# Performance work log

Hardware: AMD Instinct MI355X
Metric: run time of the kernel (lower is better)

The kernel has to match this reference:

```python
import jax, jax.numpy as jnp
import numpy as np

K = 32            # config.k: active latents per token (batch top-k)
THRESHOLD_LR = 0.01
B, S, F = 8, 256, 16384


def setup_inputs() -> dict:
    key = jax.random.key(0)
    k1, k2 = jax.random.split(key)
    x = jax.random.normal(k1, (B, S, F), dtype=jnp.float32)
    token_mask = jax.random.randint(k2, (B, S), 0, 2, dtype=jnp.int32)
    threshold = jnp.zeros((), dtype=jnp.float32)  # persistent EMA buffer, init 0.0
    return {"x": x, "token_mask": token_mask, "threshold": threshold}


def reference(x, token_mask, threshold):
    # Training path of BatchTopKActivationFunction.forward
    b, s, f = x.shape
    num_tokens = b * s
    k_total = K * num_tokens
    neg_min = jnp.finfo(x.dtype).min
    # mask out tokens: x[~token_mask] = finfo.min (so they never enter top-k)
    xm = jnp.where(token_mask.astype(bool)[:, :, None], x, neg_min)
    flat = xm.reshape(-1)                       # [b*s*f]
    vals, idx = jax.lax.top_k(flat, k_total)    # global top-k over flattened tensor
    # scatter relu'd top-k values back into a zero tensor
    result = jnp.zeros_like(flat).at[idx].set(jax.nn.relu(vals)).reshape(b, s, f)
    # EMA threshold update: min of strictly-positive selected values
    pos = vals > 0
    min_pos = jnp.min(jnp.where(pos, vals, jnp.inf))
    new_threshold = jnp.where(
        jnp.any(pos),
        (1.0 - THRESHOLD_LR) * threshold + THRESHOLD_LR * min_pos,
        threshold,
    )
    return result, new_threshold
```

## Files before the change

### kernel.cpp

```cpp
#include <hip/hip_runtime.h>

#define N_ELEMS  33554432
#define N4       8388608
#define N_TOKENS 2048
#define F4       4096
#define K_TOTAL  65536u
#define NBINS    4096

#define C_NG       4096
#define C_WINTH    4097
#define C_CANDTH   4098
#define C_NEED     4099
#define C_FB       4100
#define C_N2       4101
#define N_CTR_END  4160

#define GLIST_OFF  8192u
#define CAPG       4194304u
#define LIST2_OFF  (GLIST_OFF + 2u*CAPG)
#define CAP2       4096u
#define FB1_OFF    16777216u
#define CAPF       2097152u
#define FB2_OFF    (FB1_OFF + 2u*CAPF)

__device__ __forceinline__ unsigned keyOf(float f) {
    unsigned b = __float_as_uint(f);
    return b ^ ((unsigned)((int)b >> 31) | 0x80000000u);
}
__device__ __forceinline__ float valOf(unsigned u) {
    unsigned b = (u & 0x80000000u) ? (u ^ 0x80000000u) : ~u;
    return __uint_as_float(b);
}
__device__ __forceinline__ unsigned umaxu(unsigned a, unsigned b) { return a > b ? a : b; }

__global__ void k_init(unsigned* __restrict__ ws) {
    int t = blockIdx.x * 256 + threadIdx.x;
    if (t < N_CTR_END) ws[t] = 0u;
}

#define GBUF 1024
__global__ __launch_bounds__(512) void k_hist(const float4* __restrict__ x,
                                              const int* __restrict__ mask,
                                              unsigned* __restrict__ ws,
                                              float4* __restrict__ out) {
    __shared__ unsigned lh[NBINS];
    __shared__ uint2 sbuf[GBUF];
    __shared__ unsigned s_cnt, s_base;
    const int tok = blockIdx.x;
    float4* ot = out + (size_t)tok * F4;
    const float4 z = make_float4(0.f, 0.f, 0.f, 0.f);
    if (!mask[tok]) {
        for (int j = threadIdx.x; j < F4; j += 512) ot[j] = z;
        return;
    }
    for (int b = threadIdx.x; b < NBINS; b += 512) lh[b] = 0u;
    if (threadIdx.x == 0) s_cnt = 0u;
    __syncthreads();
    uint2* glist = (uint2*)(ws + GLIST_OFF);
    const float4* xt = x + (size_t)tok * F4;
    const unsigned baseIdx = (unsigned)tok * 16384u;
    for (int j = threadIdx.x; j < F4; j += 512) {
        float4 v = xt[j];
        ot[j] = z;
        float fv[4] = {v.x, v.y, v.z, v.w};
        #pragma unroll
        for (int c = 0; c < 4; c++) {
            float f = fv[c];
            if (f >= 2.0f) {
                unsigned u = keyOf(f);
                unsigned bin = (u - 0xC0000000u) >> 12;
                if (bin > 4095u) bin = 4095u;
                atomicAdd(&lh[bin], 1u);
                unsigned slot = atomicAdd(&s_cnt, 1u);
                uint2 e = make_uint2(u, baseIdx + (unsigned)j * 4u + (unsigned)c);
                if (slot < GBUF) sbuf[slot] = e;
                else { unsigned g = atomicAdd(&ws[C_NG], 1u); if (g < CAPG) glist[g] = e; }
            }
        }
    }
    __syncthreads();
    for (int b = threadIdx.x; b < NBINS; b += 512) {
        unsigned c = lh[b];
        if (c) atomicAdd(&ws[b], c);
    }
    unsigned cnt = s_cnt; if (cnt > GBUF) cnt = GBUF;
    if (threadIdx.x == 0) s_base = atomicAdd(&ws[C_NG], cnt);
    __syncthreads();
    for (unsigned j = threadIdx.x; j < cnt; j += 512) {
        unsigned p = s_base + j;
        if (p < CAPG) glist[p] = sbuf[j];
    }
}

__global__ __launch_bounds__(1024) void k_scan1(unsigned* __restrict__ ws) {
    __shared__ unsigned sc[1024];
    __shared__ unsigned sB1, sKA, sFound;
    const int t = threadIdx.x;
    unsigned vv[4];
    unsigned s = 0u;
    #pragma unroll
    for (int j = 0; j < 4; ++j) { vv[j] = ws[t * 4 + j]; s += vv[j]; }
    if (t == 0) sFound = 0u;
    sc[t] = s;
    __syncthreads();
    for (int off = 1; off < 1024; off <<= 1) {
        unsigned a = sc[t];
        unsigned b = (t + off < 1024) ? sc[t + off] : 0u;
        __syncthreads();
        sc[t] = a + b;
        __syncthreads();
    }
    unsigned run = (t < 1023) ? sc[t + 1] : 0u;
    #pragma unroll
    for (int j = 3; j >= 0; --j) {
        unsigned prev = run; run += vv[j];
        if (run >= K_TOTAL && prev < K_TOTAL) {
            sB1 = (unsigned)(t * 4 + j); sKA = prev; sFound = 1u;
        }
    }
    __syncthreads();
    if (t == 0) {
        unsigned total = sc[0];
        unsigned ng = ws[C_NG];
        unsigned fb = (sFound == 0u) || (total < K_TOTAL) || (sB1 == 4095u) || (ng > CAPG);
        ws[C_FB] = fb ? 1u : 0u;
        if (!fb) {
            unsigned candTh = 0xC0000000u + (sB1 << 12);
            ws[C_CANDTH] = candTh;
            ws[C_WINTH]  = candTh + 0x1000u;
            ws[C_NEED]   = K_TOTAL - sKA;
        }
    }
}

__global__ __launch_bounds__(256) void k_scatter(unsigned* __restrict__ ws,
                                                 float* __restrict__ out) {
    if (ws[C_FB]) return;
    const unsigned winTh = ws[C_WINTH], candTh = ws[C_CANDTH];
    unsigned ng = ws[C_NG]; if (ng > CAPG) ng = CAPG;
    uint2* glist = (uint2*)(ws + GLIST_OFF);
    uint2* list2 = (uint2*)(ws + LIST2_OFF);
    const unsigned stride = gridDim.x * 256;
    for (unsigned i = blockIdx.x * 256 + threadIdx.x; i < ng; i += stride) {
        uint2 e = glist[i];
        if (e.x >= winTh) out[e.y] = valOf(e.x);
        else if (e.x >= candTh) {
            unsigned g = atomicAdd(&ws[C_N2], 1u);
            if (g < CAP2) list2[g] = e;
        }
    }
}

__global__ __launch_bounds__(256) void k_tail(unsigned* __restrict__ ws,
                                              float* __restrict__ out,
                                              const float* __restrict__ thr) {
    if (ws[C_FB]) return;
    __shared__ uint2 ent[CAP2];
    __shared__ unsigned sred[256];
    const int t = threadIdx.x;
    unsigned rawn2 = ws[C_N2];
    if (rawn2 > CAP2) { if (t == 0) ws[C_FB] = 1u; return; }
    const unsigned n2 = rawn2;
    const unsigned need = ws[C_NEED];
    uint2* list2 = (uint2*)(ws + LIST2_OFF);
    for (unsigned i = t; i < n2; i += 256) ent[i] = list2[i];
    __syncthreads();
    unsigned minSel = 0xFFFFFFFFu;
    for (unsigned i = t; i < n2; i += 256) {
        uint2 e = ent[i];
        unsigned rank = 0u;
        for (unsigned j = 0; j < n2; ++j) {
            uint2 o = ent[j];
            rank += (o.x > e.x || (o.x == e.x && o.y < e.y)) ? 1u : 0u;
        }
        if (rank < need) {
            out[e.y] = valOf(e.x);
            if (e.x < minSel) minSel = e.x;
        }
    }
    sred[t] = minSel;
    __syncthreads();
    for (int off = 128; off > 0; off >>= 1) {
        if (t < off) sred[t] = sred[t] < sred[t + off] ? sred[t] : sred[t + off];
        __syncthreads();
    }
    if (t == 0) {
        out[N_ELEMS] = 0.99f * thr[0] + 0.01f * valOf(sred[0]);
    }
}

__global__ __launch_bounds__(1024) void k_fallback(const float4* __restrict__ x,
                                                   const int* __restrict__ mask,
                                                   unsigned* __restrict__ ws,
                                                   float* __restrict__ out,
                                                   const float* __restrict__ thr) {
    if (ws[C_FB] == 0u) return;
    __shared__ unsigned lh[NBINS];
    __shared__ unsigned sred[1024];
    __shared__ unsigned sB1, sKA, sMode, sNegmin, sB2, sNeed, sCnt;
    const int t = threadIdx.x;
    for (int b = t; b < NBINS; b += 1024) lh[b] = 0u;
    __syncthreads();
    unsigned negmin = 0u;
    for (int tok = 0; tok < N_TOKENS; ++tok) {
        if (!mask[tok]) continue;
        const float4* xt = x + (size_t)tok * F4;
        for (int j = t; j < F4; j += 1024) {
            float4 v = xt[j];
            float fv[4] = {v.x, v.y, v.z, v.w};
            #pragma unroll
            for (int c = 0; c < 4; ++c) {
                float f = fv[c];
                unsigned u = keyOf(f);
                atomicAdd(&lh[u >> 20], 1u);
                if (f > 0.0f) negmin = umaxu(negmin, ~u);
            }
        }
    }
    __syncthreads();
    sred[t] = negmin; __syncthreads();
    for (int off = 512; off > 0; off >>= 1) {
        if (t < off) sred[t] = umaxu(sred[t], sred[t + off]);
        __syncthreads();
    }
    if (t == 0) {
        sNegmin = sred[0];
        unsigned tot = 0u;
        for (int b = 0; b < NBINS; ++b) tot += lh[b];
        if (tot <= K_TOTAL) sMode = 1u;
        else {
            sMode = 0u;
            unsigned run = 0u, prev = 0u; int b1 = 0;
            for (int b = NBINS - 1; b >= 0; --b) {
                prev = run; run += lh[b];
                if (run >= K_TOTAL && prev < K_TOTAL) { b1 = b; break; }
            }
            sB1 = (unsigned)b1; sKA = prev;
        }
        sCnt = 0u;
    }
    __syncthreads();
    if (sMode == 1u) {
        for (int tok = 0; tok < N_TOKENS; ++tok) {
            if (!mask[tok]) continue;
            const float4* xt = x + (size_t)tok * F4;
            float* ot = out + (size_t)tok * 16384;
            for (int j = t; j < F4; j += 1024) {
                float4 v = xt[j];
                ot[j * 4 + 0] = fmaxf(v.x, 0.f); ot[j * 4 + 1] = fmaxf(v.y, 0.f);
                ot[j * 4 + 2] = fmaxf(v.z, 0.f); ot[j * 4 + 3] = fmaxf(v.w, 0.f);
            }
        }
        if (t == 0) {
            float th = thr[0], newt = th;
            if (sNegmin) newt = 0.99f * th + 0.01f * valOf(~sNegmin);
            out[N_ELEMS] = newt;
        }
        return;
    }
    const unsigned B1c = sB1;
    uint2* fb1 = (uint2*)(ws + FB1_OFF);
    for (int tok = 0; tok < N_TOKENS; ++tok) {
        if (!mask[tok]) continue;
        const float4* xt = x + (size_t)tok * F4;
        const unsigned baseIdx = (unsigned)tok * 16384u;
        for (int j = t; j < F4; j += 1024) {
            float4 v = xt[j];
            float fv[4] = {v.x, v.y, v.z, v.w};
            #pragma unroll
            for (int c = 0; c < 4; ++c) {
                float f = fv[c];
                unsigned u = keyOf(f);
                unsigned p = u >> 20;
                unsigned idx = baseIdx + (unsigned)j * 4u + (unsigned)c;
                if (p > B1c) out[idx] = fmaxf(f, 0.f);
                else if (p == B1c) {
                    unsigned g = atomicAdd(&sCnt, 1u);
                    if (g < CAPF) fb1[g] = make_uint2(u, idx);
                }
            }
        }
    }
    __syncthreads();
    unsigned n1 = sCnt > CAPF ? CAPF : sCnt;
    __syncthreads();
    if (t < 256) lh[t] = 0u;
    if (t == 0) sCnt = 0u;
    __syncthreads();
    for (unsigned i = t; i < n1; i += 1024)
        atomicAdd(&lh[(fb1[i].x >> 12) & 255u], 1u);
    __syncthreads();
    if (t == 0) {
        unsigned run = sKA, prev = sKA; int b2 = 0;
        for (int b = 255; b >= 0; --b) {
            prev = run; run += lh[b];
            if (run >= K_TOTAL) { b2 = b; break; }
        }
        sB2 = (unsigned)b2; sNeed = K_TOTAL - prev;
    }
    __syncthreads();
    const unsigned B2 = sB2, need = sNeed;
    uint2* fb2 = (uint2*)(ws + FB2_OFF);
    for (unsigned i = t; i < n1; i += 1024) {
        uint2 e = fb1[i];
        unsigned bb = (e.x >> 12) & 255u;
        if (bb > B2) out[e.y] = fmaxf(valOf(e.x), 0.f);
        else if (bb == B2) {
            unsigned g = atomicAdd(&sCnt, 1u);
            if (g < CAPF) fb2[g] = e;
        }
    }
    __syncthreads();
    unsigned n2 = sCnt > CAPF ? CAPF : sCnt;
    unsigned minSel = 0xFFFFFFFFu;
    for (unsigned i = t; i < n2; i += 1024) {
        uint2 e = fb2[i];
        unsigned rank = 0u;
        for (unsigned jj = 0; jj < n2; ++jj) {
            uint2 o = fb2[jj];
            rank += (o.x > e.x || (o.x == e.x && o.y < e.y)) ? 1u : 0u;
        }
        if (rank < need) { out[e.y] = fmaxf(valOf(e.x), 0.f); if (e.x < minSel) minSel = e.x; }
    }
    __syncthreads();
    sred[t] = minSel; __syncthreads();
    for (int off = 512; off > 0; off >>= 1) {
        if (t < off) sred[t] = sred[t] < sred[t + off] ? sred[t] : sred[t + off];
        __syncthreads();
    }
    if (t == 0) {
        float th = thr[0], newt = th;
        unsigned vku = sred[0];
        if (vku != 0xFFFFFFFFu) {
            float vk = valOf(vku);
            float minpos; int any;
            if (vk > 0.f) { minpos = vk; any = 1; }
            else { any = (sNegmin != 0u); minpos = any ? valOf(~sNegmin) : 0.f; }
            if (any) newt = 0.99f * th + 0.01f * minpos;
        }
        out[N_ELEMS] = newt;
    }
}

extern "C" void kernel_launch(void* const* d_in, const int* in_sizes, int n_in,
                              void* d_out, int out_size, void* d_ws, size_t ws_size,
                              hipStream_t stream) {
    const float4* x  = (const float4*)d_in[0];
    const int* mask  = (const int*)d_in[1];
    const float* thr = (const float*)d_in[2];
    float* out       = (float*)d_out;
    unsigned* ws     = (unsigned*)d_ws;

    k_init    <<<17, 256, 0, stream>>>(ws);
    k_hist    <<<N_TOKENS, 512, 0, stream>>>(x, mask, ws, (float4*)out);
    k_scan1   <<<1, 1024, 0, stream>>>(ws);
    k_scatter <<<256, 256, 0, stream>>>(ws, out);
    k_tail    <<<1, 256, 0, stream>>>(ws, out, thr);
    k_fallback<<<1, 1024, 0, stream>>>(x, mask, ws, out, thr);
}
```

Baseline: 272.9 us.

## Use nontemporal zero stores, skip sub-threshold vectors, merge tail and fallback kernels

The histogram pass now writes the zeroed output with nontemporal stores to avoid polluting cache, and checks the max of each float4 before running the per-element candidate logic. The tail and fallback kernels are merged into one 1024-thread launch, which drops one kernel launch and widens the tail rank computation from 256 to 1024 threads. The fallback path is unchanged in function but now shares the merged kernel's shared memory footprint.

```diff
diff --git a/kernel.cpp b/kernel.cpp
--- a/kernel.cpp
+++ b/kernel.cpp
@@ -1,7 +1,6 @@
 #include <hip/hip_runtime.h>
 
 #define N_ELEMS  33554432
-#define N4       8388608
 #define N_TOKENS 2048
 #define F4       4096
 #define K_TOTAL  65536u
@@ -22,6 +21,8 @@
 #define FB1_OFF    16777216u
 #define CAPF       2097152u
 #define FB2_OFF    (FB1_OFF + 2u*CAPF)
+
+typedef float v4f __attribute__((ext_vector_type(4)));
 
 __device__ __forceinline__ unsigned keyOf(float f) {
     unsigned b = __float_as_uint(f);
@@ -47,10 +48,11 @@
     __shared__ uint2 sbuf[GBUF];
     __shared__ unsigned s_cnt, s_base;
     const int tok = blockIdx.x;
-    float4* ot = out + (size_t)tok * F4;
-    const float4 z = make_float4(0.f, 0.f, 0.f, 0.f);
+    v4f* ot = (v4f*)(out + (size_t)tok * F4);
+    const v4f z = {0.f, 0.f, 0.f, 0.f};
     if (!mask[tok]) {
-        for (int j = threadIdx.x; j < F4; j += 512) ot[j] = z;
+        for (int j = threadIdx.x; j < F4; j += 512)
+            __builtin_nontemporal_store(z, &ot[j]);
         return;
     }
     for (int b = threadIdx.x; b < NBINS; b += 512) lh[b] = 0u;
@@ -61,20 +63,22 @@
     const unsigned baseIdx = (unsigned)tok * 16384u;
     for (int j = threadIdx.x; j < F4; j += 512) {
         float4 v = xt[j];
-        ot[j] = z;
-        float fv[4] = {v.x, v.y, v.z, v.w};
-        #pragma unroll
-        for (int c = 0; c < 4; c++) {
-            float f = fv[c];
-            if (f >= 2.0f) {
-                unsigned u = keyOf(f);
-                unsigned bin = (u - 0xC0000000u) >> 12;
-                if (bin > 4095u) bin = 4095u;
-                atomicAdd(&lh[bin], 1u);
-                unsigned slot = atomicAdd(&s_cnt, 1u);
-                uint2 e = make_uint2(u, baseIdx + (unsigned)j * 4u + (unsigned)c);
-                if (slot < GBUF) sbuf[slot] = e;
-                else { unsigned g = atomicAdd(&ws[C_NG], 1u); if (g < CAPG) glist[g] = e; }
+        __builtin_nontemporal_store(z, &ot[j]);
+        if (fmaxf(fmaxf(v.x, v.y), fmaxf(v.z, v.w)) >= 2.0f) {
+            float fv[4] = {v.x, v.y, v.z, v.w};
+            #pragma unroll
+            for (int c = 0; c < 4; c++) {
+                float f = fv[c];
+                if (f >= 2.0f) {
+                    unsigned u = keyOf(f);
+                    unsigned bin = (u - 0xC0000000u) >> 12;
+                    if (bin > 4095u) bin = 4095u;
+                    atomicAdd(&lh[bin], 1u);
+                    unsigned slot = atomicAdd(&s_cnt, 1u);
+                    uint2 e = make_uint2(u, baseIdx + (unsigned)j * 4u + (unsigned)c);
+                    if (slot < GBUF) sbuf[slot] = e;
+                    else { unsigned g = atomicAdd(&ws[C_NG], 1u); if (g < CAPG) glist[g] = e; }
+                }
             }
         }
     }
@@ -151,54 +155,51 @@
     }
 }
 
-__global__ __launch_bounds__(256) void k_tail(unsigned* __restrict__ ws,
-                                              float* __restrict__ out,
-                                              const float* __restrict__ thr) {
-    if (ws[C_FB]) return;
+__global__ __launch_bounds__(1024) void k_tailfb(const float4* __restrict__ x,
+                                                 const int* __restrict__ mask,
+                                                 unsigned* __restrict__ ws,
+                                                 float* __restrict__ out,
+                                                 const float* __restrict__ thr) {
+    __shared__ unsigned lh[NBINS];
     __shared__ uint2 ent[CAP2];
-    __shared__ unsigned sred[256];
-    const int t = threadIdx.x;
-    unsigned rawn2 = ws[C_N2];
-    if (rawn2 > CAP2) { if (t == 0) ws[C_FB] = 1u; return; }
-    const unsigned n2 = rawn2;
-    const unsigned need = ws[C_NEED];
-    uint2* list2 = (uint2*)(ws + LIST2_OFF);
-    for (unsigned i = t; i < n2; i += 256) ent[i] = list2[i];
-    __syncthreads();
-    unsigned minSel = 0xFFFFFFFFu;
-    for (unsigned i = t; i < n2; i += 256) {
-        uint2 e = ent[i];
-        unsigned rank = 0u;
-        for (unsigned j = 0; j < n2; ++j) {
-            uint2 o = ent[j];
-            rank += (o.x > e.x || (o.x == e.x && o.y < e.y)) ? 1u : 0u;
-        }
-        if (rank < need) {
-            out[e.y] = valOf(e.x);
-            if (e.x < minSel) minSel = e.x;
-        }
-    }
-    sred[t] = minSel;
-    __syncthreads();
-    for (int off = 128; off > 0; off >>= 1) {
-        if (t < off) sred[t] = sred[t] < sred[t + off] ? sred[t] : sred[t + off];
-        __syncthreads();
-    }
-    if (t == 0) {
-        out[N_ELEMS] = 0.99f * thr[0] + 0.01f * valOf(sred[0]);
-    }
-}
-
-__global__ __launch_bounds__(1024) void k_fallback(const float4* __restrict__ x,
-                                                   const int* __restrict__ mask,
-                                                   unsigned* __restrict__ ws,
-                                                   float* __restrict__ out,
-                                                   const float* __restrict__ thr) {
-    if (ws[C_FB] == 0u) return;
-    __shared__ unsigned lh[NBINS];
     __shared__ unsigned sred[1024];
     __shared__ unsigned sB1, sKA, sMode, sNegmin, sB2, sNeed, sCnt;
     const int t = threadIdx.x;
+    unsigned fb = ws[C_FB];
+
+    if (!fb) {
+        unsigned rawn2 = ws[C_N2];
+        if (rawn2 <= CAP2) {
+            const unsigned n2 = rawn2;
+            const unsigned need = ws[C_NEED];
+            uint2* list2 = (uint2*)(ws + LIST2_OFF);
+            for (unsigned i = t; i < n2; i += 1024) ent[i] = list2[i];
+            __syncthreads();
+            unsigned minSel = 0xFFFFFFFFu;
+            for (unsigned i = t; i < n2; i += 1024) {
+                uint2 e = ent[i];
+                unsigned rank = 0u;
+                for (unsigned j = 0; j < n2; ++j) {
+                    uint2 o = ent[j];
+                    rank += (o.x > e.x || (o.x == e.x && o.y < e.y)) ? 1u : 0u;
+                }
+                if (rank < need) {
+                    out[e.y] = valOf(e.x);
+                    if (e.x < minSel) minSel = e.x;
+                }
+            }
+            sred[t] = minSel;
+            __syncthreads();
+            for (int off = 512; off > 0; off >>= 1) {
+                if (t < off) sred[t] = sred[t] < sred[t + off] ? sred[t] : sred[t + off];
+                __syncthreads();
+            }
+            if (t == 0)
+                out[N_ELEMS] = 0.99f * thr[0] + 0.01f * valOf(sred[0]);
+            return;
+        }
+    }
+
     for (int b = t; b < NBINS; b += 1024) lh[b] = 0u;
     __syncthreads();
     unsigned negmin = 0u;
@@ -311,12 +312,12 @@
         }
     }
     __syncthreads();
-    unsigned n2 = sCnt > CAPF ? CAPF : sCnt;
+    unsigned n2f = sCnt > CAPF ? CAPF : sCnt;
     unsigned minSel = 0xFFFFFFFFu;
-    for (unsigned i = t; i < n2; i += 1024) {
+    for (unsigned i = t; i < n2f; i += 1024) {
         uint2 e = fb2[i];
         unsigned rank = 0u;
-        for (unsigned jj = 0; jj < n2; ++jj) {
+        for (unsigned jj = 0; jj < n2f; ++jj) {
             uint2 o = fb2[jj];
             rank += (o.x > e.x || (o.x == e.x && o.y < e.y)) ? 1u : 0u;
         }
@@ -351,10 +352,9 @@
     float* out       = (float*)d_out;
     unsigned* ws     = (unsigned*)d_ws;
 
-    k_init    <<<17, 256, 0, stream>>>(ws);
-    k_hist    <<<N_TOKENS, 512, 0, stream>>>(x, mask, ws, (float4*)out);
-    k_scan1   <<<1, 1024, 0, stream>>>(ws);
-    k_scatter <<<256, 256, 0, stream>>>(ws, out);
-    k_tail    <<<1, 256, 0, stream>>>(ws, out, thr);
-    k_fallback<<<1, 1024, 0, stream>>>(x, mask, ws, out, thr);
-}
+    k_init   <<<17, 256, 0, stream>>>(ws);
+    k_hist   <<<N_TOKENS, 512, 0, stream>>>(x, mask, ws, (float4*)out);
+    k_scan1  <<<1, 1024, 0, stream>>>(ws);
+    k_scatter<<<256, 256, 0, stream>>>(ws, out);
+    k_tailfb <<<1, 1024, 0, stream>>>(x, mask, ws, out, thr);
+}
```

Result: no change. 273.7 us (+0.3%).
